# Kernel tuning notes

Measured on AMD Instinct MI355X. Metric: run time of the kernel, lower is better.

Reference implementation:

```python
import jax, jax.numpy as jnp
import numpy as np

VOCAB = 100000
SHORTLIST = 10000  # cutoffs = [10000, 20000, 40000, 80000], n_clusters = 4
B, T, D = 1024, 128, 1024


def setup_inputs() -> dict:
    key = jax.random.key(0)
    ks = jax.random.split(key, 12)
    s = 0.02  # realistic init scale for weights
    inp = {
        "features": jax.random.normal(ks[0], (B, D), jnp.float32),
        "head_weight": jax.random.normal(ks[1], (SHORTLIST + 4, D), jnp.float32) * s,
        "proj0": jax.random.normal(ks[2], (512, D), jnp.float32) * s,
        "out0": jax.random.normal(ks[3], (10000, 512), jnp.float32) * s,
        "proj1": jax.random.normal(ks[4], (256, D), jnp.float32) * s,
        "out1": jax.random.normal(ks[5], (20000, 256), jnp.float32) * s,
        "proj2": jax.random.normal(ks[6], (128, D), jnp.float32) * s,
        "out2": jax.random.normal(ks[7], (40000, 128), jnp.float32) * s,
        "proj3": jax.random.normal(ks[8], (64, D), jnp.float32) * s,
        "out3": jax.random.normal(ks[9], (20000, 64), jnp.float32) * s,
        "discard_probs": jax.random.uniform(ks[10], (VOCAB,), jnp.float32),
        "targets": jax.random.randint(ks[11], (B, T), 0, VOCAB, jnp.int64),
        "target_mask": jnp.ones((B, T), jnp.bool_),
    }
    return inp


def _adaptive_log_prob(x, head_weight, projs, outs):
    # head: shortlist logits + one logit per tail cluster
    head_lp = jax.nn.log_softmax(x @ head_weight.T, axis=-1)  # [B, SHORTLIST+4]
    parts = [head_lp[:, :SHORTLIST]]
    for i, (pw, ow) in enumerate(zip(projs, outs)):
        cluster_logits = (x @ pw.T) @ ow.T  # [B, osz]
        parts.append(jax.nn.log_softmax(cluster_logits, axis=-1)
                     + head_lp[:, SHORTLIST + i:SHORTLIST + i + 1])
    return jnp.concatenate(parts, axis=-1)  # [B, VOCAB]


def reference(features, head_weight, proj0, out0, proj1, out1, proj2, out2,
              proj3, out3, discard_probs, targets, target_mask):
    # dropout is identity in eval/reference mode
    logprob = _adaptive_log_prob(features, head_weight,
                                 (proj0, proj1, proj2, proj3),
                                 (out0, out1, out2, out3))
    lp_t = jnp.take_along_axis(logprob, targets, axis=1)        # [B, T]
    w = (1.0 - discard_probs[targets]) * target_mask.astype(lp_t.dtype)
    per_sample = jnp.sum(-lp_t * w, axis=1) / jnp.sum(w, axis=1)  # [B]
    return jnp.sum(per_sample) / (targets.shape[0] + 1e-5)
```

## Files before the change

### kernel.cpp

```cpp
#include <hip/hip_runtime.h>
#include <cstdint>


typedef unsigned short u16;
typedef __attribute__((ext_vector_type(4))) float f32x4;
typedef __attribute__((ext_vector_type(8))) __bf16 bf16x8;
typedef __attribute__((ext_vector_type(4))) unsigned int u32x4;

__device__ __forceinline__ u16 f2bf(float f){
  unsigned u = __float_as_uint(f);
  u += 0x7FFFu + ((u >> 16) & 1u);
  return (u16)(u >> 16);
}

__device__ __forceinline__ float wave_sum(float v){
  #pragma unroll
  for (int d = 1; d < 64; d <<= 1) v += __shfl_xor(v, d, 64);
  return v;
}

__device__ __forceinline__ float wave_dot_l(const u16* a_lds, const u16* b, int len, int lane){
  float s = 0.f;
  for (int k = lane*8; k < len; k += 512){
    u32x4 va = *(const u32x4*)(a_lds + k);
    u32x4 vb = *(const u32x4*)(b + k);
    #pragma unroll
    for (int i = 0; i < 4; i++){
      unsigned ua = va[i], ub = vb[i];
      s = fmaf(__uint_as_float(ua << 16),        __uint_as_float(ub << 16),        s);
      s = fmaf(__uint_as_float(ua & 0xFFFF0000u), __uint_as_float(ub & 0xFFFF0000u), s);
    }
  }
  return wave_sum(s);
}

struct CvtSeg { const float* src; u16* dst; unsigned start; };
struct CvtTab { CvtSeg s[10]; unsigned total; };

__global__ __launch_bounds__(256) void cvt_bf16(CvtTab t){
  unsigned stride = gridDim.x * blockDim.x;
  for (unsigned c = blockIdx.x*blockDim.x + threadIdx.x; c < t.total; c += stride){
    int si = 0;
    #pragma unroll
    for (int i = 1; i < 10; i++) if (c >= t.s[i].start) si = i;
    unsigned lo = c - t.s[si].start;
    const float4* sp = (const float4*)t.s[si].src + (size_t)lo*2;
    float4 f0 = sp[0], f1 = sp[1];
    uint4 d;
    d.x = (unsigned)f2bf(f0.x) | ((unsigned)f2bf(f0.y) << 16);
    d.y = (unsigned)f2bf(f0.z) | ((unsigned)f2bf(f0.w) << 16);
    d.z = (unsigned)f2bf(f1.x) | ((unsigned)f2bf(f1.y) << 16);
    d.w = (unsigned)f2bf(f1.z) | ((unsigned)f2bf(f1.w) << 16);
    ((uint4*)t.s[si].dst)[lo] = d;
  }
}

struct GSeg { const u16* A; const u16* B; float* part; u16* C; float* gates;
              int lda, N, K, ntiles, tileStart, ldc; };
struct GTab { GSeg seg[5]; int nseg; };

__global__ __launch_bounds__(256, 3) void gemm_all(GTab tab){
  __shared__ u16 ldsA[128*64];
  __shared__ u16 ldsB[128*64];
  __shared__ float msLds[128][2];

  int by = blockIdx.y;
  int s = 0;
  #pragma unroll
  for (int i = 1; i < 5; i++)
    if (i < tab.nseg && by >= tab.seg[i].tileStart) s = i;
  const u16* Ab = tab.seg[s].A;
  const u16* Bb = tab.seg[s].B;
  float* part   = tab.seg[s].part;
  u16* Cc       = tab.seg[s].C;
  float* gatesp = tab.seg[s].gates;
  int lda = tab.seg[s].lda, N = tab.seg[s].N, K = tab.seg[s].K;
  int ntiles = tab.seg[s].ntiles, ldc = tab.seg[s].ldc;
  int tileN = by - tab.seg[s].tileStart;
  int n0 = tileN * 128;
  int row0 = blockIdx.x * 128;

  int tid = threadIdx.x;
  int wid = tid >> 6, lane = tid & 63;
  int wr = wid >> 1, wc = wid & 1;
  int qr = lane >> 4, ln = lane & 15;

  const char* baseA = (const char*)(Ab + (size_t)row0*lda);
  const char* baseB = (const char*)Bb;
  unsigned offA[4], offB[4];
  #pragma unroll
  for (int t = 0; t < 4; t++){
    int c = t*256 + tid, row = c >> 3, jj = (c & 7) ^ (row & 7);
    offA[t] = (unsigned)(row*lda + jj*8) * 2u;
    int nr = n0 + row; if (nr >= N) nr = N - 1;
    offB[t] = (unsigned)(nr*K + jj*8) * 2u;
  }

  u32x4 pa[4], pb[4];
  #pragma unroll
  for (int t = 0; t < 4; t++){ pa[t] = *(const u32x4*)(baseA + offA[t]);
                               pb[t] = *(const u32x4*)(baseB + offB[t]); }

  f32x4 acc[4][4];
  const f32x4 zero = {0.f, 0.f, 0.f, 0.f};
  #pragma unroll
  for (int i = 0; i < 4; i++)
    #pragma unroll
    for (int j = 0; j < 4; j++) acc[i][j] = zero;

  int nkt = K >> 6;
  for (int kt = 0; kt < nkt; kt++){
    __syncthreads();
    #pragma unroll
    for (int t = 0; t < 4; t++){
      *(u32x4*)((char*)ldsA + (size_t)(t*256 + tid)*16) = pa[t];
      *(u32x4*)((char*)ldsB + (size_t)(t*256 + tid)*16) = pb[t];
    }
    __syncthreads();
    if (kt + 1 < nkt){
      unsigned kb = (unsigned)(kt + 1) * 128u;
      #pragma unroll
      for (int t = 0; t < 4; t++){ pa[t] = *(const u32x4*)(baseA + offA[t] + kb);
                                   pb[t] = *(const u32x4*)(baseB + offB[t] + kb); }
    }
    #pragma unroll
    for (int ks = 0; ks < 2; ks++){
      bf16x8 av[4], bv[4];
      #pragma unroll
      for (int mt = 0; mt < 4; mt++){
        int rl = wr*64 + mt*16 + ln;
        int ch = rl*8 + ((ks*4 + qr) ^ (rl & 7));
        av[mt] = *(const bf16x8*)((const char*)ldsA + ch*16);
      }
      #pragma unroll
      for (int nt = 0; nt < 4; nt++){
        int rl = wc*64 + nt*16 + ln;
        int ch = rl*8 + ((ks*4 + qr) ^ (rl & 7));
        bv[nt] = *(const bf16x8*)((const char*)ldsB + ch*16);
      }
      #pragma unroll
      for (int mt = 0; mt < 4; mt++)
        #pragma unroll
        for (int nt = 0; nt < 4; nt++)
          acc[mt][nt] = __builtin_amdgcn_mfma_f32_16x16x32_bf16(av[mt], bv[nt], acc[mt][nt], 0, 0, 0);
    }
  }

  if (part){
    #pragma unroll
    for (int mt = 0; mt < 4; mt++){
      #pragma unroll
      for (int r = 0; r < 4; r++){
        float ss = 0.f;
        #pragma unroll
        for (int nt = 0; nt < 4; nt++){
          int col = n0 + wc*64 + nt*16 + ln;
          if (col < N){
            float v = acc[mt][nt][r];
            ss += __expf(v);
            if (gatesp && col >= 10000){
              int row = row0 + wr*64 + mt*16 + qr*4 + r;
              gatesp[row*4 + (col - 10000)] = v;
            }
          }
        }
        ss += __shfl_xor(ss, 1, 64);
        ss += __shfl_xor(ss, 2, 64);
        ss += __shfl_xor(ss, 4, 64);
        ss += __shfl_xor(ss, 8, 64);
        if (ln == 0) msLds[wr*64 + mt*16 + qr*4 + r][wc] = ss;
      }
    }
    __syncthreads();
    if (tid < 128)
      part[(size_t)(row0 + tid)*ntiles + tileN] = msLds[tid][0] + msLds[tid][1];
  } else {
    #pragma unroll
    for (int mt = 0; mt < 4; mt++)
      #pragma unroll
      for (int nt = 0; nt < 4; nt++)
        #pragma unroll
        for (int r = 0; r < 4; r++){
          int col = n0 + wc*64 + nt*16 + ln;
          if (col < N){
            int row = row0 + wr*64 + mt*16 + qr*4 + r;
            Cc[(size_t)row*ldc + col] = f2bf(acc[mt][nt][r]);
          }
        }
  }
}

struct LseTab { const float* base[5]; int ntiles[5]; float* lse; };

__global__ __launch_bounds__(256) void lse_reduce(LseTab t){
  int widx = blockIdx.x*4 + (threadIdx.x >> 6);
  int lane = threadIdx.x & 63;
  int mat = widx >> 10, row = widx & 1023;
  const float* p = t.base[mat] + (size_t)row * t.ntiles[mat];
  float s = 0.f;
  for (int i = lane; i < t.ntiles[mat]; i += 64) s += p[i];
  s = wave_sum(s);
  if (lane == 0) t.lse[mat*1024 + row] = __logf(s);
}

struct GatherArgs {
  const u16* Xb; const u16* Hb; const u16* Hact; const u16* Ob;
  const float* lse; const float* gates; const int* targets; float* lp;
};

__global__ __launch_bounds__(256) void gather_rows(GatherArgs g){
  __shared__ u16 xr[1024];
  __shared__ u16 hr[960];
  __shared__ int tg[128];
  __shared__ float ls[5], gs[4];

  int b = blockIdx.x;
  int tid = threadIdx.x;
  int w = tid >> 6, lane = tid & 63;

  if (tid < 128) ((u32x4*)xr)[tid] = ((const u32x4*)(g.Xb + (size_t)b*1024))[tid];
  else if (tid < 248) ((u32x4*)hr)[tid-128] = ((const u32x4*)(g.Hact + (size_t)b*960))[tid-128];
  if (tid < 32) ((u32x4*)tg)[tid] = ((const u32x4*)(g.targets + (size_t)b*128))[tid];
  if (tid < 5) ls[tid] = g.lse[tid*1024 + b];
  if (tid < 4) gs[tid] = g.gates[b*4 + tid];
  __syncthreads();

  for (int t = 0; t < 32; t++){
    int ti = w*32 + t;
    int v = tg[ti];
    float val;
    if (v < 10000){
      float logit = wave_dot_l(xr, g.Hb + (size_t)v*1024, 1024, lane);
      val = logit - ls[0];
    } else {
      int c, off, psz, hoff; size_t oboff;
      if      (v < 20000){ c=0; off=10000; psz=512; hoff=0;   oboff=0; }
      else if (v < 40000){ c=1; off=20000; psz=256; hoff=512; oboff=5120000; }
      else if (v < 80000){ c=2; off=40000; psz=128; hoff=768; oboff=10240000; }
      else               { c=3; off=80000; psz=64;  hoff=896; oboff=15360000; }
      float logit = wave_dot_l(hr + hoff, g.Ob + oboff + (size_t)(v - off)*psz, psz, lane);
      val = gs[c] - ls[0] + logit - ls[c + 1];
    }
    if (lane == 0) g.lp[b*128 + ti] = val;
  }
}

__global__ __launch_bounds__(128) void row_loss(const float* lp, const int* targets,
                                                const float* discard, float* psamp){
  int b = blockIdx.x, t = threadIdx.x;
  int idx = b*128 + t;
  int v = targets[idx];
  float w = 1.0f - discard[v];
  float a = -lp[idx] * w;
  float as = wave_sum(a), ws = wave_sum(w);
  __shared__ float sa[2], sw[2];
  int wid = t >> 6, lane = t & 63;
  if (lane == 0){ sa[wid] = as; sw[wid] = ws; }
  __syncthreads();
  if (t == 0) psamp[b] = (sa[0] + sa[1]) / (sw[0] + sw[1]);
}

__global__ __launch_bounds__(256) void final_sum(const float* psamp, float* out){
  float s = 0.f;
  for (int i = threadIdx.x; i < 1024; i += 256) s += psamp[i];
  s = wave_sum(s);
  __shared__ float sb[4];
  if ((threadIdx.x & 63) == 0) sb[threadIdx.x >> 6] = s;
  __syncthreads();
  if (threadIdx.x == 0) out[0] = (sb[0] + sb[1] + sb[2] + sb[3]) / (1024.0f + 1e-5f);
}

extern "C" void kernel_launch(void* const* d_in, const int* in_sizes, int n_in,
                              void* d_out, int out_size, void* d_ws, size_t ws_size,
                              hipStream_t stream){
  (void)in_sizes; (void)n_in; (void)out_size; (void)ws_size;
  const float* features = (const float*)d_in[0];
  const float* head_w   = (const float*)d_in[1];
  const float* proj[4]  = {(const float*)d_in[2], (const float*)d_in[4],
                           (const float*)d_in[6], (const float*)d_in[8]};
  const float* outw[4]  = {(const float*)d_in[3], (const float*)d_in[5],
                           (const float*)d_in[7], (const float*)d_in[9]};
  const float* discard  = (const float*)d_in[10];
  const int*   targets  = (const int*)d_in[11];
  float* out = (float*)d_out;

  char* wsp = (char*)d_ws;
  size_t off = 0;
  auto carve = [&](size_t bytes)->char*{
    char* p = wsp + off; off += (bytes + 255) & ~(size_t)255; return p;
  };
  u16* Xb     = (u16*)carve(1024ull*1024*2);
  u16* Hb     = (u16*)carve(10004ull*1024*2);
  u16* Pb     = (u16*)carve(960ull*1024*2);
  u16* Ob     = (u16*)carve(16640000ull*2);
  u16* Hact   = (u16*)carve(1024ull*960*2);
  float* part = (float*)carve(803840ull*4);
  float* lse  = (float*)carve(5*1024*4);
  float* gates= (float*)carve(4096*4);
  float* lp   = (float*)carve(131072ull*4);
  float* psamp= (float*)carve(1024*4);

  CvtTab ct{};
  const float* srcs[10] = {features, head_w, proj[0], proj[1], proj[2], proj[3],
                           outw[0], outw[1], outw[2], outw[3]};
  u16* dsts[10] = {Xb, Hb, Pb, Pb + 512*1024, Pb + 768*1024, Pb + 896*1024,
                   Ob, Ob + 5120000, Ob + 10240000, Ob + 15360000};
  unsigned counts[10] = {1048576u, 10244096u, 524288u, 262144u, 131072u, 65536u,
                         5120000u, 5120000u, 5120000u, 1280000u};
  unsigned pre = 0;
  for (int i = 0; i < 10; i++){
    ct.s[i].src = srcs[i]; ct.s[i].dst = dsts[i]; ct.s[i].start = pre;
    pre += counts[i] / 8;
  }
  ct.total = pre;
  cvt_bf16<<<dim3(4096), dim3(256), 0, stream>>>(ct);

  float* pHead = part;
  float* pC0 = part + 80896;
  float* pC1 = part + 161792;
  float* pC2 = part + 322560;
  float* pC3 = part + 643072;

  GTab tp{};
  tp.nseg = 4;
  tp.seg[0] = {Xb, Pb,            nullptr, Hact,       nullptr, 1024, 512, 1024, 4, 0, 960};
  tp.seg[1] = {Xb, Pb + 512*1024, nullptr, Hact + 512, nullptr, 1024, 256, 1024, 2, 4, 960};
  tp.seg[2] = {Xb, Pb + 768*1024, nullptr, Hact + 768, nullptr, 1024, 128, 1024, 1, 6, 960};
  tp.seg[3] = {Xb, Pb + 896*1024, nullptr, Hact + 896, nullptr, 1024, 64,  1024, 1, 7, 960};
  gemm_all<<<dim3(8, 8), dim3(256), 0, stream>>>(tp);

  GTab tm{};
  tm.nseg = 5;
  tm.seg[0] = {Xb,         Hb,            pHead, nullptr, gates,   1024, 10004, 1024, 79,  0,   0};
  tm.seg[1] = {Hact,       Ob,            pC0,   nullptr, nullptr, 960,  10000, 512,  79,  79,  0};
  tm.seg[2] = {Hact + 512, Ob + 5120000,  pC1,   nullptr, nullptr, 960,  20000, 256,  157, 158, 0};
  tm.seg[3] = {Hact + 768, Ob + 10240000, pC2,   nullptr, nullptr, 960,  40000, 128,  313, 315, 0};
  tm.seg[4] = {Hact + 896, Ob + 15360000, pC3,   nullptr, nullptr, 960,  20000, 64,   157, 628, 0};
  gemm_all<<<dim3(8, 785), dim3(256), 0, stream>>>(tm);

  LseTab lt{};
  lt.base[0] = pHead; lt.base[1] = pC0; lt.base[2] = pC1; lt.base[3] = pC2; lt.base[4] = pC3;
  lt.ntiles[0] = 79; lt.ntiles[1] = 79; lt.ntiles[2] = 157; lt.ntiles[3] = 313; lt.ntiles[4] = 157;
  lt.lse = lse;
  lse_reduce<<<dim3(1280), dim3(256), 0, stream>>>(lt);

  GatherArgs ga{Xb, Hb, Hact, Ob, lse, gates, targets, lp};
  gather_rows<<<dim3(1024), dim3(256), 0, stream>>>(ga);

  row_loss<<<dim3(1024), dim3(128), 0, stream>>>(lp, targets, discard, psamp);
  final_sum<<<dim3(1), dim3(256), 0, stream>>>(psamp, out);
}
```

Measured before the change: 314.9 us.

## Fuse fp32-to-bf16 conversion into GEMM loads and remap tiles per XCD

Removes the separate conversion kernel that wrote bf16 copies of every weight and the features. The GEMM now reads fp32 weights and features directly and rounds them to bf16 while staging into LDS, and the gather step uses fp32 weights. It also moves to a 1D grid with a tile index mapping that keeps the 8 row-blocks of one N-tile on the same XCD, so they can share L2. This saves a full read and write pass over roughly 90 MB of weights, but the GEMM now loads twice as many bytes for B, and it uses more registers and does extra pack work inside the main loop.

```diff
diff --git a/kernel.cpp b/kernel.cpp
--- a/kernel.cpp
+++ b/kernel.cpp
@@ -13,93 +13,108 @@
   return (u16)(u >> 16);
 }
 
+__device__ __forceinline__ unsigned rhu2(unsigned a, unsigned b){
+  return ((a + 0x8000u) >> 16) | ((b + 0x8000u) & 0xFFFF0000u);
+}
+__device__ __forceinline__ u32x4 pack8(u32x4 lo, u32x4 hi){
+  u32x4 r;
+  r[0] = rhu2(lo[0], lo[1]); r[1] = rhu2(lo[2], lo[3]);
+  r[2] = rhu2(hi[0], hi[1]); r[3] = rhu2(hi[2], hi[3]);
+  return r;
+}
+
 __device__ __forceinline__ float wave_sum(float v){
   #pragma unroll
   for (int d = 1; d < 64; d <<= 1) v += __shfl_xor(v, d, 64);
   return v;
 }
 
-__device__ __forceinline__ float wave_dot_l(const u16* a_lds, const u16* b, int len, int lane){
+__device__ __forceinline__ float wave_dot_ff(const float* a, const float* b, int len, int lane){
   float s = 0.f;
   for (int k = lane*8; k < len; k += 512){
-    u32x4 va = *(const u32x4*)(a_lds + k);
-    u32x4 vb = *(const u32x4*)(b + k);
-    #pragma unroll
-    for (int i = 0; i < 4; i++){
-      unsigned ua = va[i], ub = vb[i];
-      s = fmaf(__uint_as_float(ua << 16),        __uint_as_float(ub << 16),        s);
-      s = fmaf(__uint_as_float(ua & 0xFFFF0000u), __uint_as_float(ub & 0xFFFF0000u), s);
-    }
+    float4 a0 = *(const float4*)(a + k), a1 = *(const float4*)(a + k + 4);
+    float4 b0 = *(const float4*)(b + k), b1 = *(const float4*)(b + k + 4);
+    s = fmaf(a0.x,b0.x, fmaf(a0.y,b0.y, fmaf(a0.z,b0.z, fmaf(a0.w,b0.w, s))));
+    s = fmaf(a1.x,b1.x, fmaf(a1.y,b1.y, fmaf(a1.z,b1.z, fmaf(a1.w,b1.w, s))));
   }
   return wave_sum(s);
 }
-
-struct CvtSeg { const float* src; u16* dst; unsigned start; };
-struct CvtTab { CvtSeg s[10]; unsigned total; };
-
-__global__ __launch_bounds__(256) void cvt_bf16(CvtTab t){
-  unsigned stride = gridDim.x * blockDim.x;
-  for (unsigned c = blockIdx.x*blockDim.x + threadIdx.x; c < t.total; c += stride){
-    int si = 0;
-    #pragma unroll
-    for (int i = 1; i < 10; i++) if (c >= t.s[i].start) si = i;
-    unsigned lo = c - t.s[si].start;
-    const float4* sp = (const float4*)t.s[si].src + (size_t)lo*2;
-    float4 f0 = sp[0], f1 = sp[1];
-    uint4 d;
-    d.x = (unsigned)f2bf(f0.x) | ((unsigned)f2bf(f0.y) << 16);
-    d.y = (unsigned)f2bf(f0.z) | ((unsigned)f2bf(f0.w) << 16);
-    d.z = (unsigned)f2bf(f1.x) | ((unsigned)f2bf(f1.y) << 16);
-    d.w = (unsigned)f2bf(f1.z) | ((unsigned)f2bf(f1.w) << 16);
-    ((uint4*)t.s[si].dst)[lo] = d;
-  }
-}
-
-struct GSeg { const u16* A; const u16* B; float* part; u16* C; float* gates;
-              int lda, N, K, ntiles, tileStart, ldc; };
-struct GTab { GSeg seg[5]; int nseg; };
+__device__ __forceinline__ float wave_dot_hf(const u16* a, const float* b, int len, int lane){
+  float s = 0.f;
+  for (int k = lane*8; k < len; k += 512){
+    u32x4 va = *(const u32x4*)(a + k);
+    float4 b0 = *(const float4*)(b + k), b1 = *(const float4*)(b + k + 4);
+    s = fmaf(__uint_as_float(va[0] << 16),        b0.x, s);
+    s = fmaf(__uint_as_float(va[0] & 0xFFFF0000u), b0.y, s);
+    s = fmaf(__uint_as_float(va[1] << 16),        b0.z, s);
+    s = fmaf(__uint_as_float(va[1] & 0xFFFF0000u), b0.w, s);
+    s = fmaf(__uint_as_float(va[2] << 16),        b1.x, s);
+    s = fmaf(__uint_as_float(va[2] & 0xFFFF0000u), b1.y, s);
+    s = fmaf(__uint_as_float(va[3] << 16),        b1.z, s);
+    s = fmaf(__uint_as_float(va[3] & 0xFFFF0000u), b1.w, s);
+  }
+  return wave_sum(s);
+}
+
+struct GSeg { const void* A; const float* B; float* part; u16* C; float* gates;
+              int lda, N, K, ntiles, tileStart, ldc, abf16; };
+struct GTab { GSeg seg[5]; int nseg; int ntotal; };
 
 __global__ __launch_bounds__(256, 3) void gemm_all(GTab tab){
   __shared__ u16 ldsA[128*64];
   __shared__ u16 ldsB[128*64];
   __shared__ float msLds[128][2];
 
-  int by = blockIdx.y;
+  int id = blockIdx.x;
+  int xcd = id & 7, sl = id >> 3;
+  int t = (sl >> 3)*8 + xcd;
+  int mblk = sl & 7;
+  if (t >= tab.ntotal) return;
+
   int s = 0;
   #pragma unroll
   for (int i = 1; i < 5; i++)
-    if (i < tab.nseg && by >= tab.seg[i].tileStart) s = i;
-  const u16* Ab = tab.seg[s].A;
-  const u16* Bb = tab.seg[s].B;
-  float* part   = tab.seg[s].part;
-  u16* Cc       = tab.seg[s].C;
-  float* gatesp = tab.seg[s].gates;
-  int lda = tab.seg[s].lda, N = tab.seg[s].N, K = tab.seg[s].K;
-  int ntiles = tab.seg[s].ntiles, ldc = tab.seg[s].ldc;
-  int tileN = by - tab.seg[s].tileStart;
+    if (i < tab.nseg && t >= tab.seg[i].tileStart) s = i;
+  const GSeg& sg = tab.seg[s];
+  const float* Bb = sg.B;
+  float* part   = sg.part;
+  u16* Cc       = sg.C;
+  float* gatesp = sg.gates;
+  int lda = sg.lda, N = sg.N, K = sg.K;
+  int ntiles = sg.ntiles, ldc = sg.ldc;
+  int abf16 = sg.abf16;
+  int tileN = t - sg.tileStart;
   int n0 = tileN * 128;
-  int row0 = blockIdx.x * 128;
+  int row0 = mblk * 128;
 
   int tid = threadIdx.x;
   int wid = tid >> 6, lane = tid & 63;
   int wr = wid >> 1, wc = wid & 1;
   int qr = lane >> 4, ln = lane & 15;
 
-  const char* baseA = (const char*)(Ab + (size_t)row0*lda);
+  const char* baseA = (const char*)sg.A + (((size_t)row0*lda) << (abf16 ? 1 : 2));
   const char* baseB = (const char*)Bb;
   unsigned offA[4], offB[4];
   #pragma unroll
-  for (int t = 0; t < 4; t++){
-    int c = t*256 + tid, row = c >> 3, jj = (c & 7) ^ (row & 7);
-    offA[t] = (unsigned)(row*lda + jj*8) * 2u;
+  for (int t4 = 0; t4 < 4; t4++){
+    int c = t4*256 + tid, row = c >> 3, jj = (c & 7) ^ (row & 7);
+    offA[t4] = ((unsigned)(row*lda + jj*8)) << (abf16 ? 1 : 2);
     int nr = n0 + row; if (nr >= N) nr = N - 1;
-    offB[t] = (unsigned)(nr*K + jj*8) * 2u;
-  }
-
-  u32x4 pa[4], pb[4];
-  #pragma unroll
-  for (int t = 0; t < 4; t++){ pa[t] = *(const u32x4*)(baseA + offA[t]);
-                               pb[t] = *(const u32x4*)(baseB + offB[t]); }
+    offB[t4] = ((unsigned)(nr*K + jj*8)) << 2;
+  }
+
+  u32x4 pa[4], pa2[4], pb[4], pb2[4];
+  #pragma unroll
+  for (int t4 = 0; t4 < 4; t4++){
+    if (abf16){
+      pa[t4] = *(const u32x4*)(baseA + offA[t4]);
+    } else {
+      pa[t4]  = *(const u32x4*)(baseA + offA[t4]);
+      pa2[t4] = *(const u32x4*)(baseA + offA[t4] + 16);
+    }
+    pb[t4]  = *(const u32x4*)(baseB + offB[t4]);
+    pb2[t4] = *(const u32x4*)(baseB + offB[t4] + 16);
+  }
 
   f32x4 acc[4][4];
   const f32x4 zero = {0.f, 0.f, 0.f, 0.f};
@@ -109,19 +124,30 @@
     for (int j = 0; j < 4; j++) acc[i][j] = zero;
 
   int nkt = K >> 6;
+  unsigned stepA = abf16 ? 128u : 256u;
   for (int kt = 0; kt < nkt; kt++){
     __syncthreads();
     #pragma unroll
-    for (int t = 0; t < 4; t++){
-      *(u32x4*)((char*)ldsA + (size_t)(t*256 + tid)*16) = pa[t];
-      *(u32x4*)((char*)ldsB + (size_t)(t*256 + tid)*16) = pb[t];
+    for (int t4 = 0; t4 < 4; t4++){
+      u32x4 wa = abf16 ? pa[t4] : pack8(pa[t4], pa2[t4]);
+      *(u32x4*)((char*)ldsA + (size_t)(t4*256 + tid)*16) = wa;
+      *(u32x4*)((char*)ldsB + (size_t)(t4*256 + tid)*16) = pack8(pb[t4], pb2[t4]);
     }
     __syncthreads();
     if (kt + 1 < nkt){
-      unsigned kb = (unsigned)(kt + 1) * 128u;
-      #pragma unroll
-      for (int t = 0; t < 4; t++){ pa[t] = *(const u32x4*)(baseA + offA[t] + kb);
-                                   pb[t] = *(const u32x4*)(baseB + offB[t] + kb); }
+      unsigned kbA = (unsigned)(kt + 1) * stepA;
+      unsigned kbB = (unsigned)(kt + 1) * 256u;
+      #pragma unroll
+      for (int t4 = 0; t4 < 4; t4++){
+        if (abf16){
+          pa[t4] = *(const u32x4*)(baseA + offA[t4] + kbA);
+        } else {
+          pa[t4]  = *(const u32x4*)(baseA + offA[t4] + kbA);
+          pa2[t4] = *(const u32x4*)(baseA + offA[t4] + kbA + 16);
+        }
+        pb[t4]  = *(const u32x4*)(baseB + offB[t4] + kbB);
+        pb2[t4] = *(const u32x4*)(baseB + offB[t4] + kbB + 16);
+      }
     }
     #pragma unroll
     for (int ks = 0; ks < 2; ks++){
@@ -204,12 +230,13 @@
 }
 
 struct GatherArgs {
-  const u16* Xb; const u16* Hb; const u16* Hact; const u16* Ob;
+  const float* Xf; const float* Hw; const u16* Hact;
+  const float* Ow0; const float* Ow1; const float* Ow2; const float* Ow3;
   const float* lse; const float* gates; const int* targets; float* lp;
 };
 
 __global__ __launch_bounds__(256) void gather_rows(GatherArgs g){
-  __shared__ u16 xr[1024];
+  __shared__ float xr[1024];
   __shared__ u16 hr[960];
   __shared__ int tg[128];
   __shared__ float ls[5], gs[4];
@@ -218,8 +245,8 @@
   int tid = threadIdx.x;
   int w = tid >> 6, lane = tid & 63;
 
-  if (tid < 128) ((u32x4*)xr)[tid] = ((const u32x4*)(g.Xb + (size_t)b*1024))[tid];
-  else if (tid < 248) ((u32x4*)hr)[tid-128] = ((const u32x4*)(g.Hact + (size_t)b*960))[tid-128];
+  ((float4*)xr)[tid] = ((const float4*)(g.Xf + (size_t)b*1024))[tid];
+  if (tid < 120) ((u32x4*)hr)[tid] = ((const u32x4*)(g.Hact + (size_t)b*960))[tid];
   if (tid < 32) ((u32x4*)tg)[tid] = ((const u32x4*)(g.targets + (size_t)b*128))[tid];
   if (tid < 5) ls[tid] = g.lse[tid*1024 + b];
   if (tid < 4) gs[tid] = g.gates[b*4 + tid];
@@ -230,15 +257,15 @@
     int v = tg[ti];
     float val;
     if (v < 10000){
-      float logit = wave_dot_l(xr, g.Hb + (size_t)v*1024, 1024, lane);
+      float logit = wave_dot_ff(xr, g.Hw + (size_t)v*1024, 1024, lane);
       val = logit - ls[0];
     } else {
-      int c, off, psz, hoff; size_t oboff;
-      if      (v < 20000){ c=0; off=10000; psz=512; hoff=0;   oboff=0; }
-      else if (v < 40000){ c=1; off=20000; psz=256; hoff=512; oboff=5120000; }
-      else if (v < 80000){ c=2; off=40000; psz=128; hoff=768; oboff=10240000; }
-      else               { c=3; off=80000; psz=64;  hoff=896; oboff=15360000; }
-      float logit = wave_dot_l(hr + hoff, g.Ob + oboff + (size_t)(v - off)*psz, psz, lane);
+      int c, off, psz, hoff; const float* Ow;
+      if      (v < 20000){ c=0; off=10000; psz=512; hoff=0;   Ow=g.Ow0; }
+      else if (v < 40000){ c=1; off=20000; psz=256; hoff=512; Ow=g.Ow1; }
+      else if (v < 80000){ c=2; off=40000; psz=128; hoff=768; Ow=g.Ow2; }
+      else               { c=3; off=80000; psz=64;  hoff=896; Ow=g.Ow3; }
+      float logit = wave_dot_hf(hr + hoff, Ow + (size_t)(v - off)*psz, psz, lane);
       val = gs[c] - ls[0] + logit - ls[c + 1];
     }
     if (lane == 0) g.lp[b*128 + ti] = val;
@@ -289,10 +316,6 @@
   auto carve = [&](size_t bytes)->char*{
     char* p = wsp + off; off += (bytes + 255) & ~(size_t)255; return p;
   };
-  u16* Xb     = (u16*)carve(1024ull*1024*2);
-  u16* Hb     = (u16*)carve(10004ull*1024*2);
-  u16* Pb     = (u16*)carve(960ull*1024*2);
-  u16* Ob     = (u16*)carve(16640000ull*2);
   u16* Hact   = (u16*)carve(1024ull*960*2);
   float* part = (float*)carve(803840ull*4);
   float* lse  = (float*)carve(5*1024*4);
@@ -300,21 +323,6 @@
   float* lp   = (float*)carve(131072ull*4);
   float* psamp= (float*)carve(1024*4);
 
-  CvtTab ct{};
-  const float* srcs[10] = {features, head_w, proj[0], proj[1], proj[2], proj[3],
-                           outw[0], outw[1], outw[2], outw[3]};
-  u16* dsts[10] = {Xb, Hb, Pb, Pb + 512*1024, Pb + 768*1024, Pb + 896*1024,
-                   Ob, Ob + 5120000, Ob + 10240000, Ob + 15360000};
-  unsigned counts[10] = {1048576u, 10244096u, 524288u, 262144u, 131072u, 65536u,
-                         5120000u, 5120000u, 5120000u, 1280000u};
-  unsigned pre = 0;
-  for (int i = 0; i < 10; i++){
-    ct.s[i].src = srcs[i]; ct.s[i].dst = dsts[i]; ct.s[i].start = pre;
-    pre += counts[i] / 8;
-  }
-  ct.total = pre;
-  cvt_bf16<<<dim3(4096), dim3(256), 0, stream>>>(ct);
-
   float* pHead = part;
   float* pC0 = part + 80896;
   float* pC1 = part + 161792;
@@ -322,21 +330,21 @@
   float* pC3 = part + 643072;
 
   GTab tp{};
-  tp.nseg = 4;
-  tp.seg[0] = {Xb, Pb,            nullptr, Hact,       nullptr, 1024, 512, 1024, 4, 0, 960};
-  tp.seg[1] = {Xb, Pb + 512*1024, nullptr, Hact + 512, nullptr, 1024, 256, 1024, 2, 4, 960};
-  tp.seg[2] = {Xb, Pb + 768*1024, nullptr, Hact + 768, nullptr, 1024, 128, 1024, 1, 6, 960};
-  tp.seg[3] = {Xb, Pb + 896*1024, nullptr, Hact + 896, nullptr, 1024, 64,  1024, 1, 7, 960};
-  gemm_all<<<dim3(8, 8), dim3(256), 0, stream>>>(tp);
+  tp.nseg = 4; tp.ntotal = 8;
+  tp.seg[0] = {features, proj[0], nullptr, Hact,       nullptr, 1024, 512, 1024, 4, 0, 960, 0};
+  tp.seg[1] = {features, proj[1], nullptr, Hact + 512, nullptr, 1024, 256, 1024, 2, 4, 960, 0};
+  tp.seg[2] = {features, proj[2], nullptr, Hact + 768, nullptr, 1024, 128, 1024, 1, 6, 960, 0};
+  tp.seg[3] = {features, proj[3], nullptr, Hact + 896, nullptr, 1024, 64,  1024, 1, 7, 960, 0};
+  gemm_all<<<dim3(64), dim3(256), 0, stream>>>(tp);
 
   GTab tm{};
-  tm.nseg = 5;
-  tm.seg[0] = {Xb,         Hb,            pHead, nullptr, gates,   1024, 10004, 1024, 79,  0,   0};
-  tm.seg[1] = {Hact,       Ob,            pC0,   nullptr, nullptr, 960,  10000, 512,  79,  79,  0};
-  tm.seg[2] = {Hact + 512, Ob + 5120000,  pC1,   nullptr, nullptr, 960,  20000, 256,  157, 158, 0};
-  tm.seg[3] = {Hact + 768, Ob + 10240000, pC2,   nullptr, nullptr, 960,  40000, 128,  313, 315, 0};
-  tm.seg[4] = {Hact + 896, Ob + 15360000, pC3,   nullptr, nullptr, 960,  20000, 64,   157, 628, 0};
-  gemm_all<<<dim3(8, 785), dim3(256), 0, stream>>>(tm);
+  tm.nseg = 5; tm.ntotal = 785;
+  tm.seg[0] = {features,   head_w,  pHead, nullptr, gates,   1024, 10004, 1024, 79,  0,   0, 0};
+  tm.seg[1] = {Hact,       outw[0], pC0,   nullptr, nullptr, 960,  10000, 512,  79,  79,  0, 1};
+  tm.seg[2] = {Hact + 512, outw[1], pC1,   nullptr, nullptr, 960,  20000, 256,  157, 158, 0, 1};
+  tm.seg[3] = {Hact + 768, outw[2], pC2,   nullptr, nullptr, 960,  40000, 128,  313, 315, 0, 1};
+  tm.seg[4] = {Hact + 896, outw[3], pC3,   nullptr, nullptr, 960,  20000, 64,   157, 628, 0, 1};
+  gemm_all<<<dim3(8*8*99), dim3(256), 0, stream>>>(tm);
 
   LseTab lt{};
   lt.base[0] = pHead; lt.base[1] = pC0; lt.base[2] = pC1; lt.base[3] = pC2; lt.base[4] = pC3;
@@ -344,7 +352,8 @@
   lt.lse = lse;
   lse_reduce<<<dim3(1280), dim3(256), 0, stream>>>(lt);
 
-  GatherArgs ga{Xb, Hb, Hact, Ob, lse, gates, targets, lp};
+  GatherArgs ga{features, head_w, Hact, outw[0], outw[1], outw[2], outw[3],
+                lse, gates, targets, lp};
   gather_rows<<<dim3(1024), dim3(256), 0, stream>>>(ga);
 
   row_loss<<<dim3(1024), dim3(128), 0, stream>>>(lp, targets, discard, psamp);
```

Result: slower. 359.2 us (+14.0%).

## Remap GEMM blocks to XCD-aware 1D grid and reuse LDS for row sums

Applied to the files above, without the earlier changes.

Changes the 2D grid to a 1D grid whose block index is decoded so that the 8 M-blocks sharing one N-tile of weights run on the same XCD. The goal is to reuse the B tile in that XCD's L2 instead of fetching it from several XCDs. It also moves the row-sum scratch into the existing ldsA buffer, guarded by an extra barrier, and raises launch bounds occupancy from 3 to 5 blocks. Padding the grid to 8*8*99 adds a few early-exit blocks, and the higher occupancy target may cause register spills.

```diff
diff --git a/kernel.cpp b/kernel.cpp
--- a/kernel.cpp
+++ b/kernel.cpp
@@ -57,18 +57,23 @@
 
 struct GSeg { const u16* A; const u16* B; float* part; u16* C; float* gates;
               int lda, N, K, ntiles, tileStart, ldc; };
-struct GTab { GSeg seg[5]; int nseg; };
-
-__global__ __launch_bounds__(256, 3) void gemm_all(GTab tab){
+struct GTab { GSeg seg[5]; int nseg; int ntotal; };
+
+__global__ __launch_bounds__(256, 5) void gemm_all(GTab tab){
   __shared__ u16 ldsA[128*64];
   __shared__ u16 ldsB[128*64];
-  __shared__ float msLds[128][2];
-
-  int by = blockIdx.y;
+  float* msLds = (float*)ldsA;
+
+  int id = blockIdx.x;
+  int xcd = id & 7, sl = id >> 3;
+  int t = (sl >> 3)*8 + xcd;
+  int mblk = sl & 7;
+  if (t >= tab.ntotal) return;
+
   int s = 0;
   #pragma unroll
   for (int i = 1; i < 5; i++)
-    if (i < tab.nseg && by >= tab.seg[i].tileStart) s = i;
+    if (i < tab.nseg && t >= tab.seg[i].tileStart) s = i;
   const u16* Ab = tab.seg[s].A;
   const u16* Bb = tab.seg[s].B;
   float* part   = tab.seg[s].part;
@@ -76,9 +81,9 @@
   float* gatesp = tab.seg[s].gates;
   int lda = tab.seg[s].lda, N = tab.seg[s].N, K = tab.seg[s].K;
   int ntiles = tab.seg[s].ntiles, ldc = tab.seg[s].ldc;
-  int tileN = by - tab.seg[s].tileStart;
+  int tileN = t - tab.seg[s].tileStart;
   int n0 = tileN * 128;
-  int row0 = blockIdx.x * 128;
+  int row0 = mblk * 128;
 
   int tid = threadIdx.x;
   int wid = tid >> 6, lane = tid & 63;
@@ -89,17 +94,17 @@
   const char* baseB = (const char*)Bb;
   unsigned offA[4], offB[4];
   #pragma unroll
-  for (int t = 0; t < 4; t++){
-    int c = t*256 + tid, row = c >> 3, jj = (c & 7) ^ (row & 7);
-    offA[t] = (unsigned)(row*lda + jj*8) * 2u;
+  for (int t4 = 0; t4 < 4; t4++){
+    int c = t4*256 + tid, row = c >> 3, jj = (c & 7) ^ (row & 7);
+    offA[t4] = (unsigned)(row*lda + jj*8) * 2u;
     int nr = n0 + row; if (nr >= N) nr = N - 1;
-    offB[t] = (unsigned)(nr*K + jj*8) * 2u;
+    offB[t4] = (unsigned)(nr*K + jj*8) * 2u;
   }
 
   u32x4 pa[4], pb[4];
   #pragma unroll
-  for (int t = 0; t < 4; t++){ pa[t] = *(const u32x4*)(baseA + offA[t]);
-                               pb[t] = *(const u32x4*)(baseB + offB[t]); }
+  for (int t4 = 0; t4 < 4; t4++){ pa[t4] = *(const u32x4*)(baseA + offA[t4]);
+                                  pb[t4] = *(const u32x4*)(baseB + offB[t4]); }
 
   f32x4 acc[4][4];
   const f32x4 zero = {0.f, 0.f, 0.f, 0.f};
@@ -112,16 +117,16 @@
   for (int kt = 0; kt < nkt; kt++){
     __syncthreads();
     #pragma unroll
-    for (int t = 0; t < 4; t++){
-      *(u32x4*)((char*)ldsA + (size_t)(t*256 + tid)*16) = pa[t];
-      *(u32x4*)((char*)ldsB + (size_t)(t*256 + tid)*16) = pb[t];
+    for (int t4 = 0; t4 < 4; t4++){
+      *(u32x4*)((char*)ldsA + (size_t)(t4*256 + tid)*16) = pa[t4];
+      *(u32x4*)((char*)ldsB + (size_t)(t4*256 + tid)*16) = pb[t4];
     }
     __syncthreads();
     if (kt + 1 < nkt){
       unsigned kb = (unsigned)(kt + 1) * 128u;
       #pragma unroll
-      for (int t = 0; t < 4; t++){ pa[t] = *(const u32x4*)(baseA + offA[t] + kb);
-                                   pb[t] = *(const u32x4*)(baseB + offB[t] + kb); }
+      for (int t4 = 0; t4 < 4; t4++){ pa[t4] = *(const u32x4*)(baseA + offA[t4] + kb);
+                                      pb[t4] = *(const u32x4*)(baseB + offB[t4] + kb); }
     }
     #pragma unroll
     for (int ks = 0; ks < 2; ks++){
@@ -147,6 +152,7 @@
   }
 
   if (part){
+    __syncthreads();
     #pragma unroll
     for (int mt = 0; mt < 4; mt++){
       #pragma unroll
@@ -168,12 +174,12 @@
         ss += __shfl_xor(ss, 2, 64);
         ss += __shfl_xor(ss, 4, 64);
         ss += __shfl_xor(ss, 8, 64);
-        if (ln == 0) msLds[wr*64 + mt*16 + qr*4 + r][wc] = ss;
+        if (ln == 0) msLds[(wr*64 + mt*16 + qr*4 + r)*2 + wc] = ss;
       }
     }
     __syncthreads();
     if (tid < 128)
-      part[(size_t)(row0 + tid)*ntiles + tileN] = msLds[tid][0] + msLds[tid][1];
+      part[(size_t)(row0 + tid)*ntiles + tileN] = msLds[tid*2] + msLds[tid*2 + 1];
   } else {
     #pragma unroll
     for (int mt = 0; mt < 4; mt++)
@@ -322,21 +328,21 @@
   float* pC3 = part + 643072;
 
   GTab tp{};
-  tp.nseg = 4;
+  tp.nseg = 4; tp.ntotal = 8;
   tp.seg[0] = {Xb, Pb,            nullptr, Hact,       nullptr, 1024, 512, 1024, 4, 0, 960};
   tp.seg[1] = {Xb, Pb + 512*1024, nullptr, Hact + 512, nullptr, 1024, 256, 1024, 2, 4, 960};
   tp.seg[2] = {Xb, Pb + 768*1024, nullptr, Hact + 768, nullptr, 1024, 128, 1024, 1, 6, 960};
   tp.seg[3] = {Xb, Pb + 896*1024, nullptr, Hact + 896, nullptr, 1024, 64,  1024, 1, 7, 960};
-  gemm_all<<<dim3(8, 8), dim3(256), 0, stream>>>(tp);
+  gemm_all<<<dim3(64), dim3(256), 0, stream>>>(tp);
 
   GTab tm{};
-  tm.nseg = 5;
+  tm.nseg = 5; tm.ntotal = 785;
   tm.seg[0] = {Xb,         Hb,            pHead, nullptr, gates,   1024, 10004, 1024, 79,  0,   0};
   tm.seg[1] = {Hact,       Ob,            pC0,   nullptr, nullptr, 960,  10000, 512,  79,  79,  0};
   tm.seg[2] = {Hact + 512, Ob + 5120000,  pC1,   nullptr, nullptr, 960,  20000, 256,  157, 158, 0};
   tm.seg[3] = {Hact + 768, Ob + 10240000, pC2,   nullptr, nullptr, 960,  40000, 128,  313, 315, 0};
   tm.seg[4] = {Hact + 896, Ob + 15360000, pC3,   nullptr, nullptr, 960,  20000, 64,   157, 628, 0};
-  gemm_all<<<dim3(8, 785), dim3(256), 0, stream>>>(tm);
+  gemm_all<<<dim3(8*8*99), dim3(256), 0, stream>>>(tm);
 
   LseTab lt{};
   lt.base[0] = pHead; lt.base[1] = pC0; lt.base[2] = pC1; lt.base[3] = pC2; lt.base[4] = pC3;
```

After: 655.2 us. 2.08x slower.
